# Performance work log

Hardware: AMD Instinct MI355X
Metric: run time of the kernel (lower is better)

## Reference

```python
import jax, jax.numpy as jnp
import numpy as np

BATCH = 16384
NUM_IN = 4096
NUM_OUT = 1024
NNZ = 262144
BN_EPS = 1e-3  # keras BatchNormalization default epsilon


def setup_inputs() -> dict:
    key = jax.random.key(0)
    ks = jax.random.split(key, 6)
    x = jax.random.normal(ks[0], (BATCH, NUM_IN), dtype=jnp.float32)
    sp_values = jax.random.normal(ks[1], (NNZ,), dtype=jnp.float32)
    gamma = jnp.ones((NUM_IN,), dtype=jnp.float32)
    beta = jnp.zeros((NUM_IN,), dtype=jnp.float32)
    moving_mean = jax.random.normal(ks[2], (NUM_IN,), dtype=jnp.float32)
    # positive moving variance in [0.5, 1.5)
    moving_var = jax.random.uniform(ks[3], (NUM_IN,), dtype=jnp.float32, minval=0.5, maxval=1.5)
    sp_rows = jax.random.randint(ks[4], (NNZ,), 0, NUM_IN, dtype=jnp.int32)
    sp_cols = jax.random.randint(ks[5], (NNZ,), 0, NUM_OUT, dtype=jnp.int32)
    return {
        "x": x,
        "sp_values": sp_values,
        "gamma": gamma,
        "beta": beta,
        "moving_mean": moving_mean,
        "moving_var": moving_var,
        "sp_rows": sp_rows,
        "sp_cols": sp_cols,
    }


def reference(x, sp_values, gamma, beta, moving_mean, moving_var, sp_rows, sp_cols):
    # BatchNorm (inference mode, moving statistics), fused elementwise
    h = (x - moving_mean) * (gamma * jax.lax.rsqrt(moving_var + BN_EPS)) + beta
    # Scatter the fixed-index sparse weights into a small dense [NUM_IN, NUM_OUT]
    # matrix (16 MB), then a single dense GEMM — honors SparseTensor semantics
    # (duplicate indices accumulate) while staying GEMM-efficient.
    W = jnp.zeros((NUM_IN, NUM_OUT), dtype=x.dtype).at[sp_rows, sp_cols].add(sp_values)
    return h @ W  # [BATCH, NUM_OUT]
```

## Files before the change

### kernel.cpp

```cpp
#include <hip/hip_runtime.h>
#include <hip/hip_bf16.h>

#define BATCH   16384
#define NUM_IN  4096
#define NUM_OUT 1024
#define NNZ     262144
#define BN_EPS  1e-3f

typedef __attribute__((ext_vector_type(8)))  short short8;
typedef __attribute__((ext_vector_type(4)))  float f32x4;
typedef __attribute__((ext_vector_type(4)))  unsigned int u32x4;

typedef __attribute__((address_space(3))) void        lds_void_t;
typedef const __attribute__((address_space(1))) void  g_void_t;

__device__ inline unsigned short f2bf(float f) {
    unsigned int u = __builtin_bit_cast(unsigned int, f);
    u += 0x7fffu + ((u >> 16) & 1u);
    return (unsigned short)(u >> 16);
}

__global__ void k_zero(f32x4* __restrict__ p) {
    p[(size_t)blockIdx.x * 256 + threadIdx.x] = f32x4{0.f, 0.f, 0.f, 0.f};
}

__global__ void k_scatter(const float* __restrict__ v, const int* __restrict__ r,
                          const int* __restrict__ c, float* __restrict__ wtf) {
    int i = blockIdx.x * 256 + threadIdx.x;
    atomicAdd(&wtf[(size_t)c[i] * NUM_IN + r[i]], v[i]);
}

__global__ void k_wprep(const float* __restrict__ wtf, const float* __restrict__ gamma,
                        const float* __restrict__ beta, const float* __restrict__ mean,
                        const float* __restrict__ var, unsigned short* __restrict__ wtb,
                        float* __restrict__ bias) {
    const int n = blockIdx.x;
    const int t = threadIdx.x;
    float acc = 0.f;
    for (int k = t; k < NUM_IN; k += 256) {
        float w = wtf[(size_t)n * NUM_IN + k];
        float s = gamma[k] * rsqrtf(var[k] + BN_EPS);
        wtb[(size_t)n * NUM_IN + k] = f2bf(w * s);
        acc += (beta[k] - mean[k] * s) * w;
    }
    #pragma unroll
    for (int o = 32; o; o >>= 1) acc += __shfl_down(acc, o, 64);
    __shared__ float red[4];
    if ((t & 63) == 0) red[t >> 6] = acc;
    __syncthreads();
    if (t == 0) bias[n] = red[0] + red[1] + red[2] + red[3];
}

#define BM 256
#define BN 256
#define BK 64
#define NT (NUM_IN / BK)
#define SLOT 65536
#define BOFF 32768

__global__ __launch_bounds__(512, 2) void k_gemm(const float* __restrict__ x,
                                                 const unsigned short* __restrict__ wt,
                                                 const float* __restrict__ bias,
                                                 float* __restrict__ out) {
    __shared__ __align__(128) char lds[2 * SLOT];

    const int bid = blockIdx.x;
    const int swz = (bid & 7) * 32 + (bid >> 3);
    const int m0 = (swz >> 2) * BM;
    const int n0 = (swz & 3) * BN;

    const int t    = threadIdx.x;
    const int lane = t & 63;
    const int wid  = t >> 6;
    const int wm   = wid >> 2;
    const int wn   = wid & 3;

    const char* xb = (const char*)x;
    const char* wb = (const char*)wt;

    const int awBase = ((t >> 2) & 1) * 16384 + (t >> 7) * 1024
                     + (((((t >> 3) & 15) | ((t & 3) << 4)) ^ (t & 7)) * 16);
    const int la0 = (lane ^ (lane >> 4)) * 16;
    const int la1 = (lane ^ ((lane >> 4) | 4)) * 16;
    const int bColB = (wn * 64 + (lane & 15)) * 128;
    const int bC0   = (((lane >> 4)    ) ^ (lane & 7)) * 16;
    const int bC1   = ((4 + (lane >> 4)) ^ (lane & 7)) * 16;

    f32x4 rc0[4], rc1[4];
    auto loadA01 = [&](int kt) {
        #pragma unroll
        for (int i = 0; i < 2; ++i) {
            const char* p = xb + (size_t)(m0 + i * 64 + (t >> 3)) * (NUM_IN * 4)
                          + (size_t)kt * (BK * 4) + (t & 7) * 32;
            rc0[2 * i]     = *(const f32x4*)(p);
            rc0[2 * i + 1] = *(const f32x4*)(p + 16);
        }
    };
    auto loadA23 = [&](int kt) {
        #pragma unroll
        for (int i = 0; i < 2; ++i) {
            const char* p = xb + (size_t)(m0 + (i + 2) * 64 + (t >> 3)) * (NUM_IN * 4)
                          + (size_t)kt * (BK * 4) + (t & 7) * 32;
            rc1[2 * i]     = *(const f32x4*)(p);
            rc1[2 * i + 1] = *(const f32x4*)(p + 16);
        }
    };
    auto convWriteA01 = [&](int sl) {
        char* dst = lds + sl * SLOT + awBase;
        #pragma unroll
        for (int i = 0; i < 2; ++i) {
            const unsigned int* f0 = (const unsigned int*)&rc0[2 * i];
            const unsigned int* f1 = (const unsigned int*)&rc0[2 * i + 1];
            u32x4 w;
            w[0] = __builtin_amdgcn_perm(f0[1], f0[0], 0x07060302u);
            w[1] = __builtin_amdgcn_perm(f0[3], f0[2], 0x07060302u);
            w[2] = __builtin_amdgcn_perm(f1[1], f1[0], 0x07060302u);
            w[3] = __builtin_amdgcn_perm(f1[3], f1[2], 0x07060302u);
            *(u32x4*)(dst + i * 4096) = w;
        }
    };
    auto convWriteA23 = [&](int sl) {
        char* dst = lds + sl * SLOT + awBase;
        #pragma unroll
        for (int i = 0; i < 2; ++i) {
            const unsigned int* f0 = (const unsigned int*)&rc1[2 * i];
            const unsigned int* f1 = (const unsigned int*)&rc1[2 * i + 1];
            u32x4 w;
            w[0] = __builtin_amdgcn_perm(f0[1], f0[0], 0x07060302u);
            w[1] = __builtin_amdgcn_perm(f0[3], f0[2], 0x07060302u);
            w[2] = __builtin_amdgcn_perm(f1[1], f1[0], 0x07060302u);
            w[3] = __builtin_amdgcn_perm(f1[3], f1[2], 0x07060302u);
            *(u32x4*)(dst + (i + 2) * 4096) = w;
        }
    };
    auto stageB = [&](int kt, int sl) {
        #pragma unroll
        for (int i = 0; i < 4; ++i) {
            int col = i * 64 + (t >> 3);
            size_t src = (size_t)(n0 + col) * (NUM_IN * 2) + (size_t)kt * (BK * 2)
                       + (((t & 7) ^ ((t >> 3) & 7)) * 16);
            __builtin_amdgcn_global_load_lds((g_void_t*)(wb + src),
                (lds_void_t*)(lds + sl * SLOT + BOFF + i * 8192 + t * 16), 16, 0, 0);
        }
    };

    short8 af[4], bf0[4], bf1[4];
    auto readA4 = [&](const char* A, int kk, int mh) {
        const char* base = A + kk * 16384 + (wm * 8 + mh * 4) * 1024
                         + (kk ? la1 : la0);
        af[0] = *(const short8*)(base);
        af[1] = *(const short8*)(base + 1024);
        af[2] = *(const short8*)(base + 2048);
        af[3] = *(const short8*)(base + 3072);
    };
    auto readB4 = [&](const char* B, int co, short8* bf) {
        const char* base = B + bColB + co;
        bf[0] = *(const short8*)(base);
        bf[1] = *(const short8*)(base + 2048);
        bf[2] = *(const short8*)(base + 4096);
        bf[3] = *(const short8*)(base + 6144);
    };

    f32x4 acc[8][4] = {};
    auto mfma16 = [&](short8* bf, int mlb) {
        __builtin_amdgcn_s_setprio(1);
        #pragma unroll
        for (int mi = 0; mi < 4; ++mi)
            #pragma unroll
            for (int nf = 0; nf < 4; ++nf)
                acc[mlb + mi][nf] = __builtin_amdgcn_mfma_f32_16x16x32_bf16(
                    af[mi], bf[nf], acc[mlb + mi][nf], 0, 0, 0);
        __builtin_amdgcn_s_setprio(0);
    };

    loadA01(0); loadA23(0);
    stageB(0, 0);
    asm volatile("s_waitcnt vmcnt(4)" ::: "memory");
    convWriteA01(0); convWriteA23(0);
    asm volatile("s_waitcnt lgkmcnt(0)" ::: "memory");
    __builtin_amdgcn_s_barrier();

    #pragma unroll 1
    for (int kt = 0; kt < NT; ++kt) {
        const int s = kt & 1;
        const char* Ap = lds + s * SLOT;
        const char* Bp = Ap + BOFF;
        const bool st = (kt + 1) < NT;
        asm volatile("s_waitcnt vmcnt(0)" ::: "memory");
        if (st) loadA01(kt + 1);
        readB4(Bp, bC0, bf0);
        readA4(Ap, 0, 0);
        __builtin_amdgcn_s_barrier();
        asm volatile("s_waitcnt lgkmcnt(0)" ::: "memory");
        __builtin_amdgcn_sched_barrier(0);
        mfma16(bf0, 0);
        __builtin_amdgcn_s_barrier();
        if (st) { loadA23(kt + 1); stageB(kt + 1, s ^ 1); }
        readA4(Ap, 0, 1);
        __builtin_amdgcn_s_barrier();
        asm volatile("s_waitcnt lgkmcnt(0)" ::: "memory");
        __builtin_amdgcn_sched_barrier(0);
        mfma16(bf0, 4);
        __builtin_amdgcn_s_barrier();
        if (st) {
            asm volatile("s_waitcnt vmcnt(8)" ::: "memory");
            convWriteA01(s ^ 1);
        }
        readB4(Bp, bC1, bf1);
        readA4(Ap, 1, 0);
        __builtin_amdgcn_s_barrier();
        asm volatile("s_waitcnt lgkmcnt(0)" ::: "memory");
        __builtin_amdgcn_sched_barrier(0);
        mfma16(bf1, 0);
        __builtin_amdgcn_s_barrier();
        if (st) {
            asm volatile("s_waitcnt vmcnt(4)" ::: "memory");
            convWriteA23(s ^ 1);
        }
        readA4(Ap, 1, 1);
        __builtin_amdgcn_s_barrier();
        asm volatile("s_waitcnt lgkmcnt(0)" ::: "memory");
        __builtin_amdgcn_sched_barrier(0);
        mfma16(bf1, 4);
        __builtin_amdgcn_s_barrier();
    }

    float bj[4];
    #pragma unroll
    for (int n = 0; n < 4; ++n) bj[n] = bias[n0 + wn * 64 + n * 16 + (lane & 15)];
    const int mb = m0 + wm * 128 + (lane >> 4) * 4;
    const int nb = n0 + wn * 64 + (lane & 15);
    #pragma unroll
    for (int ml = 0; ml < 8; ++ml)
        #pragma unroll
        for (int n = 0; n < 4; ++n)
            #pragma unroll
            for (int r = 0; r < 4; ++r)
                out[(size_t)(mb + ml * 16 + r) * NUM_OUT + (nb + n * 16)] =
                    acc[ml][n][r] + bj[n];
}

extern "C" void kernel_launch(void* const* d_in, const int* in_sizes, int n_in,
                              void* d_out, int out_size, void* d_ws, size_t ws_size,
                              hipStream_t stream) {
    const float* x     = (const float*)d_in[0];
    const float* spv   = (const float*)d_in[1];
    const float* gamma = (const float*)d_in[2];
    const float* beta  = (const float*)d_in[3];
    const float* mean  = (const float*)d_in[4];
    const float* var   = (const float*)d_in[5];
    const int*   rows  = (const int*)d_in[6];
    const int*   cols  = (const int*)d_in[7];
    float* out = (float*)d_out;

    float* wtf = (float*)d_out;
    unsigned short* wtb = (unsigned short*)d_ws;
    float* bias = (float*)((char*)d_ws + (size_t)NUM_IN * NUM_OUT * sizeof(unsigned short));

    hipLaunchKernelGGL(k_zero, dim3((NUM_IN * NUM_OUT / 4) / 256), dim3(256), 0, stream,
                       (f32x4*)wtf);
    hipLaunchKernelGGL(k_scatter, dim3(NNZ / 256), dim3(256), 0, stream,
                       spv, rows, cols, wtf);
    hipLaunchKernelGGL(k_wprep, dim3(NUM_OUT), dim3(256), 0, stream,
                       wtf, gamma, beta, mean, var, wtb, bias);
    hipLaunchKernelGGL(k_gemm, dim3((BATCH / BM) * (NUM_OUT / BN)), dim3(512), 0, stream,
                       x, wtb, bias, out);
}
```

Baseline: 215.3 us.

## Triple-buffer B tiles in LDS and prefetch two K-steps ahead

Splits LDS into a double-buffered A region and a separate triple-buffered B region, growing LDS to 160KB. B tiles are now staged via global_load_lds two iterations ahead, and the per-iteration vmcnt(0) wait at the top of the loop is dropped. The vmcnt counts are adjusted for the tail iteration. The aim is to hide global-memory latency for the weights better. The risk is that the B tile for the current step is no longer explicitly waited on before being read, and the larger LDS footprint limits the kernel to one block per CU.

```diff
diff --git a/kernel.cpp b/kernel.cpp
--- a/kernel.cpp
+++ b/kernel.cpp
@@ -55,14 +55,15 @@
 #define BN 256
 #define BK 64
 #define NT (NUM_IN / BK)
-#define SLOT 65536
-#define BOFF 32768
+#define ASL 32768
+#define BBASE 65536
+#define BSL 32768
 
 __global__ __launch_bounds__(512, 2) void k_gemm(const float* __restrict__ x,
                                                  const unsigned short* __restrict__ wt,
                                                  const float* __restrict__ bias,
                                                  float* __restrict__ out) {
-    __shared__ __align__(128) char lds[2 * SLOT];
+    __shared__ __align__(128) char lds[163840];
 
     const int bid = blockIdx.x;
     const int swz = (bid & 7) * 32 + (bid >> 3);
@@ -106,7 +107,7 @@
         }
     };
     auto convWriteA01 = [&](int sl) {
-        char* dst = lds + sl * SLOT + awBase;
+        char* dst = lds + sl * ASL + awBase;
         #pragma unroll
         for (int i = 0; i < 2; ++i) {
             const unsigned int* f0 = (const unsigned int*)&rc0[2 * i];
@@ -120,7 +121,7 @@
         }
     };
     auto convWriteA23 = [&](int sl) {
-        char* dst = lds + sl * SLOT + awBase;
+        char* dst = lds + sl * ASL + awBase;
         #pragma unroll
         for (int i = 0; i < 2; ++i) {
             const unsigned int* f0 = (const unsigned int*)&rc1[2 * i];
@@ -140,7 +141,7 @@
             size_t src = (size_t)(n0 + col) * (NUM_IN * 2) + (size_t)kt * (BK * 2)
                        + (((t & 7) ^ ((t >> 3) & 7)) * 16);
             __builtin_amdgcn_global_load_lds((g_void_t*)(wb + src),
-                (lds_void_t*)(lds + sl * SLOT + BOFF + i * 8192 + t * 16), 16, 0, 0);
+                (lds_void_t*)(lds + BBASE + sl * BSL + i * 8192 + t * 16), 16, 0, 0);
         }
     };
 
@@ -173,21 +174,23 @@
         __builtin_amdgcn_s_setprio(0);
     };
 
+    stageB(0, 0);
+    stageB(1, 1);
     loadA01(0); loadA23(0);
-    stageB(0, 0);
-    asm volatile("s_waitcnt vmcnt(4)" ::: "memory");
+    asm volatile("s_waitcnt vmcnt(0)" ::: "memory");
     convWriteA01(0); convWriteA23(0);
     asm volatile("s_waitcnt lgkmcnt(0)" ::: "memory");
     __builtin_amdgcn_s_barrier();
 
     #pragma unroll 1
     for (int kt = 0; kt < NT; ++kt) {
-        const int s = kt & 1;
-        const char* Ap = lds + s * SLOT;
-        const char* Bp = Ap + BOFF;
-        const bool st = (kt + 1) < NT;
-        asm volatile("s_waitcnt vmcnt(0)" ::: "memory");
-        if (st) loadA01(kt + 1);
+        const int s  = kt & 1;
+        const int bs = kt % 3;
+        const char* Ap = lds + s * ASL;
+        const char* Bp = lds + BBASE + bs * BSL;
+        const bool st1 = (kt + 1) < NT;
+        const bool st2 = (kt + 2) < NT;
+        if (st1) loadA01(kt + 1);
         readB4(Bp, bC0, bf0);
         readA4(Ap, 0, 0);
         __builtin_amdgcn_s_barrier();
@@ -195,15 +198,17 @@
         __builtin_amdgcn_sched_barrier(0);
         mfma16(bf0, 0);
         __builtin_amdgcn_s_barrier();
-        if (st) { loadA23(kt + 1); stageB(kt + 1, s ^ 1); }
+        if (st1) loadA23(kt + 1);
+        if (st2) stageB(kt + 2, (kt + 2) % 3);
         readA4(Ap, 0, 1);
         __builtin_amdgcn_s_barrier();
         asm volatile("s_waitcnt lgkmcnt(0)" ::: "memory");
         __builtin_amdgcn_sched_barrier(0);
         mfma16(bf0, 4);
         __builtin_amdgcn_s_barrier();
-        if (st) {
-            asm volatile("s_waitcnt vmcnt(8)" ::: "memory");
+        if (st1) {
+            if (st2) asm volatile("s_waitcnt vmcnt(8)" ::: "memory");
+            else     asm volatile("s_waitcnt vmcnt(4)" ::: "memory");
             convWriteA01(s ^ 1);
         }
         readB4(Bp, bC1, bf1);
@@ -213,8 +218,9 @@
         __builtin_amdgcn_sched_barrier(0);
         mfma16(bf1, 0);
         __builtin_amdgcn_s_barrier();
-        if (st) {
-            asm volatile("s_waitcnt vmcnt(4)" ::: "memory");
+        if (st1) {
+            if (st2) asm volatile("s_waitcnt vmcnt(4)" ::: "memory");
+            else     asm volatile("s_waitcnt vmcnt(0)" ::: "memory");
             convWriteA23(s ^ 1);
         }
         readA4(Ap, 1, 1);
```

New measurement: 217.4 us. About the same (+1.0%).
